# Kernel tuning notes

Hardware: AMD Instinct MI355X
Metric: run time of the kernel (lower is better)

The kernel has to match this reference:

```python
import jax, jax.numpy as jnp
import numpy as np
from jax import lax

SCORE_T = 0.5
NMS_T = 0.7
MAX_DET = 100
B, N = 8, 4096


def _box_cxcywh_to_xyxy(b):
    cx, cy, w, h = jnp.split(b, 4, axis=-1)
    return jnp.concatenate([cx - 0.5 * w, cy - 0.5 * h, cx + 0.5 * w, cy + 0.5 * h], axis=-1)


def _pairwise_iou(b):  # b: [N,4] xyxy -> [N,N]
    area = jnp.clip(b[:, 2] - b[:, 0], 0) * jnp.clip(b[:, 3] - b[:, 1], 0)
    lt = jnp.maximum(b[:, None, :2], b[None, :, :2])
    rb = jnp.minimum(b[:, None, 2:], b[None, :, 2:])
    wh = jnp.clip(rb - lt, 0)
    inter = wh[..., 0] * wh[..., 1]
    union = area[:, None] + area[None, :] - inter
    return inter / jnp.maximum(union, 1e-9)


def _nms_keep(iou, valid):
    # greedy NMS over score-descending order; keep[i]=True means box i survives
    n = valid.shape[0]
    idx = jnp.arange(n)

    def body(i, keep):
        sup = keep[i] & (iou[i] > NMS_T) & (idx > i)
        return keep & ~sup

    return lax.fori_loop(0, n, body, valid)


def _postprocess_image(boxes, scores):
    # boxes: [N,4] cxcywh, scores: [N]
    valid = scores > SCORE_T                       # score filter mask
    order = jnp.argsort(-jnp.where(valid, scores, -jnp.inf))  # score-descending
    bs = boxes[order]
    ss = scores[order]
    vs = valid[order]
    xyxy = _box_cxcywh_to_xyxy(bs)                 # NMS runs on xyxy boxes
    iou = _pairwise_iou(xyxy)
    keep = _nms_keep(lax.stop_gradient(iou), vs)
    kept_scores = jnp.where(keep, ss, -jnp.inf)
    top_s, top_i = lax.top_k(kept_scores, MAX_DET)  # final topk cap
    v = jnp.isfinite(top_s)
    out_boxes = bs[top_i] * v[:, None].astype(bs.dtype)  # original cxcywh boxes, zero-padded
    out_scores = jnp.where(v, top_s, 0.0)
    num = jnp.sum(v.astype(jnp.int32))
    return out_boxes, out_scores, num


def setup_inputs() -> dict:
    key = jax.random.key(0)
    k1, k2 = jax.random.split(key)
    pred_boxes = jax.random.uniform(k1, (B, N, 4), dtype=jnp.float32)
    scores = jax.random.uniform(k2, (B, N), dtype=jnp.float32)
    return {"pred_boxes": pred_boxes, "scores": scores}


def reference(pred_boxes, scores):
    out_boxes, out_scores, num = jax.vmap(_postprocess_image)(pred_boxes, scores)
    # packed [B, MAX_DET, 5]: xyxy-stage-filtered cxcywh boxes + score; num: [B]
    packed = jnp.concatenate([out_boxes, out_scores[..., None]], axis=-1)
    return packed, num
```

## Files before the change

kernel.cpp:

```cpp
#include <hip/hip_runtime.h>

#define NT 1024
#define NW 16
#define NH 4
#define NBOX 4096
#define NPT 4
#define MAXDET 100
#define KSEL 192
#define CAP 512
#define MSMALL 320

typedef unsigned long long u64;
typedef unsigned int u32;
typedef unsigned short u16;

__device__ __forceinline__ float iou_xyxy(float4 a, float4 c) {
  float aa = fmaxf(a.z - a.x, 0.f) * fmaxf(a.w - a.y, 0.f);
  float ca = fmaxf(c.z - c.x, 0.f) * fmaxf(c.w - c.y, 0.f);
  float w = fmaxf(fminf(a.z, c.z) - fmaxf(a.x, c.x), 0.f);
  float h = fmaxf(fminf(a.w, c.w) - fmaxf(a.y, c.y), 0.f);
  float inter = w * h;
  return inter / fmaxf(aa + ca - inter, 1e-9f);
}

__device__ __forceinline__ u64 wave_or64(u64 v) {
#pragma unroll
  for (int d = 1; d < 64; d <<= 1) v |= __shfl_xor(v, d);
  return v;
}

__device__ __forceinline__ u64 serial_greedy(u64 rows_mine, u64 removed) {
  u64 keep = 0ull;
  for (int ii = 0; ii < 64; ++ii) {
    u64 row = __shfl(rows_mine, ii);
    if (!((removed >> ii) & 1ull)) { keep |= 1ull << ii; removed |= row; }
  }
  return keep;
}

template <bool LDSBOX>
__device__ void run_nms128(const u64* keys, int len, const float4* __restrict__ bx,
                           const u16* sortedSlot, const float4* cbst,
                           float4* chbox, float4* chcw, u64* srowLo, u64* srowHi,
                           u64* crossM, u64* keptkey, float4* keptxy, float4* keptcw,
                           int* p_kept, int tid) {
  const int lane = tid & 63;
  for (int base = 0; base < len; base += 128) {
    if (*p_kept >= MAXDET) break;
    const int L = min(128, len - base);
    if (tid < 128) {
      if (tid < 2) crossM[tid] = 0ull;
      float4 bb = make_float4(0.f, 0.f, 0.f, 0.f);
      float4 c = make_float4(0.f, 0.f, 0.f, 0.f);
      if (tid < L) {
        if (LDSBOX) {
          c = cbst[sortedSlot[base + tid]];
        } else {
          u64 k = keys[base + tid];
          int orig = NBOX - 1 - (int)(k & 0xFFFFFFFFull);
          c = bx[orig];
        }
        bb = make_float4(c.x - 0.5f * c.z, c.y - 0.5f * c.w,
                         c.x + 0.5f * c.z, c.y + 0.5f * c.w);
      }
      chbox[tid] = bb;
      chcw[tid] = c;
      srowLo[tid] = 0ull;
      srowHi[tid] = 0ull;
    }
    __syncthreads();
    const int kept0 = *p_kept;
    {
      int i = tid & 127, slice = tid >> 7;
      if (i < L) {
        float4 a = chbox[i];
        bool hit = false;
        for (int k0 = slice; k0 < kept0 && !hit; k0 += 8)
          if (iou_xyxy(a, keptxy[k0]) > 0.7f) hit = true;
        if (hit) atomicOr(&crossM[i >> 6], 1ull << (i & 63));
        u64 blo = 0ull, bhi = 0ull;
        for (int j = i + 1 + slice; j < L; j += 8)
          if (iou_xyxy(a, chbox[j]) > 0.7f) {
            if (j < 64) blo |= 1ull << j; else bhi |= 1ull << (j - 64);
          }
        if (blo) atomicOr(&srowLo[i], blo);
        if (bhi) atomicOr(&srowHi[i], bhi);
      }
    }
    __syncthreads();
    if (tid < 64) {
      u64 remL = crossM[0], remH = crossM[1];
      if (L < 64) remL |= ~((1ull << L) - 1ull);
      if (L <= 64) remH = ~0ull;
      else if (L < 128) remH |= ~((1ull << (L - 64)) - 1ull);
      u64 rAlo = srowLo[lane], rAhi = srowHi[lane];
      u64 rBhi = srowHi[64 + lane];
      u64 K1 = ~remL;
      u64 c1 = wave_or64(((K1 >> lane) & 1ull) ? (rAlo & K1) : 0ull);
      u64 keep1 = (c1 == 0ull) ? K1 : serial_greedy(rAlo, remL);
      u64 remH2 = remH | wave_or64(((keep1 >> lane) & 1ull) ? rAhi : 0ull);
      u64 K2 = ~remH2;
      u64 c2 = wave_or64(((K2 >> lane) & 1ull) ? (rBhi & K2) : 0ull);
      u64 keep2 = (c2 == 0ull) ? K2 : serial_greedy(rBhi, remH2);
      int cnt1 = (int)__popcll(keep1);
      u64 below = (1ull << lane) - 1ull;
      if ((keep1 >> lane) & 1ull) {
        int pos = kept0 + (int)__popcll(keep1 & below);
        if (pos < MAXDET) {
          keptkey[pos] = keys[base + lane];
          keptxy[pos] = chbox[lane];
          keptcw[pos] = chcw[lane];
        }
      }
      if ((keep2 >> lane) & 1ull) {
        int pos = kept0 + cnt1 + (int)__popcll(keep2 & below);
        if (pos < MAXDET) {
          keptkey[pos] = keys[base + 64 + lane];
          keptxy[pos] = chbox[64 + lane];
          keptcw[pos] = chcw[64 + lane];
        }
      }
      if (lane == 0)
        *p_kept = min(MAXDET, kept0 + cnt1 + (int)__popcll(keep2));
    }
    __syncthreads();
  }
}

__global__ __launch_bounds__(NT) void postproc_kernel(
    const float* __restrict__ boxes,
    const float* __restrict__ scores,
    float* __restrict__ out,
    int B) {
  const int b = blockIdx.x;
  const int tid = threadIdx.x, wid = tid >> 6, lane = tid & 63;

  __shared__ u32 hist[NH][256];
  __shared__ u64 cand[CAP];
  __shared__ u64 sortedCand[CAP];
  __shared__ u16 sortedSlot[CAP];
  __shared__ float4 cbst[CAP];
  __shared__ u64 skey[NBOX];
  __shared__ float4 chbox[128];
  __shared__ float4 chcw[128];
  __shared__ u64 srowLo[128], srowHi[128];
  __shared__ u64 crossM[2];
  __shared__ float4 keptxy[MAXDET];
  __shared__ float4 keptcw[MAXDET];
  __shared__ u64 keptkey[MAXDET];
  __shared__ int s_M, s_C, s_kept, s_ovf, s_byte, s_above, s_bcnt;
  __shared__ int s_minP, s_maxP;

  const float* sc = scores + (size_t)b * NBOX;
  const float4* bx = (const float4*)boxes + (size_t)b * NBOX;

  if (tid == 0) {
    s_M = 0; s_C = 0; s_kept = 0; s_ovf = 0;
    s_minP = 0x7FFFFFFF; s_maxP = -1;
  }
  ((u32*)hist)[tid] = 0u;

  u64 key[NPT];
  {
    const int t4 = tid * NPT;
    float4 f0 = *(const float4*)(sc + t4);
    float xs[NPT] = {f0.x, f0.y, f0.z, f0.w};
    int myM = 0, pmin = 0x7FFFFFFF, pmax = -1;
#pragma unroll
    for (int q = 0; q < NPT; ++q) {
      float x = xs[q];
      bool valid = (x > 0.5f);
      u32 bits = __float_as_uint(x);
      key[q] = valid ? (((u64)bits << 32) | (u64)(u32)(NBOX - 1 - (t4 + q))) : 0ull;
      if (valid) {
        int p = (int)(bits >> 23);
        pmin = min(pmin, p); pmax = max(pmax, p); ++myM;
      }
    }
#pragma unroll
    for (int d = 1; d < 64; d <<= 1) {
      myM += __shfl_xor(myM, d);
      pmin = min(pmin, __shfl_xor(pmin, d));
      pmax = max(pmax, __shfl_xor(pmax, d));
    }
    __syncthreads();
    if (lane == 0) {
      atomicAdd(&s_M, myM);
      atomicMin(&s_minP, pmin);
      atomicMax(&s_maxP, pmax);
    }
  }
  __syncthreads();
  const int M = s_M;
  const bool uniformP = (s_minP == s_maxP);
  bool fullpath = false;
  bool usehist = false;
  u32 thr = 0;

  if (M > MSMALL) {
    if (uniformP) {
      usehist = true;
#pragma unroll
      for (int q = 0; q < NPT; ++q)
        if (key[q]) atomicAdd(&hist[wid >> 2][(u32)(key[q] >> 47) & 255u], 1u);
      __syncthreads();
      if (tid < 64) {
        int cc[4];
#pragma unroll
        for (int qq = 0; qq < 4; ++qq) {
          int bin = tid * 4 + qq;
          cc[qq] = (int)(hist[0][bin] + hist[1][bin] + hist[2][bin] + hist[3][bin]);
        }
        int tot = cc[0] + cc[1] + cc[2] + cc[3];
        int suf = tot;
#pragma unroll
        for (int d = 1; d < 64; d <<= 1) {
          int o = __shfl_down(suf, d);
          if (tid + d < 64) suf += o;
        }
        if (suf - tot < KSEL && suf >= KSEL) {
          int cum = suf - tot;
          for (int qq = 3; qq >= 0; --qq) {
            if (cum + cc[qq] >= KSEL) { s_byte = tid * 4 + qq; s_above = cum; s_bcnt = cc[qq]; break; }
            cum += cc[qq];
          }
        }
      }
      __syncthreads();
      thr = (u32)s_byte;
      if (s_above + s_bcnt > CAP) fullpath = true;
    } else {
      fullpath = true;
    }
  }

  if (!fullpath) {
#pragma unroll
    for (int q = 0; q < NPT; ++q) {
      bool take = key[q] && (!usehist || (((u32)(key[q] >> 47) & 255u) >= thr));
      u64 bal = __ballot(take);
      if (bal) {
        int leader = __ffsll((unsigned long long)bal) - 1;
        int basep = 0;
        if (lane == leader) basep = atomicAdd(&s_C, (int)__popcll(bal));
        basep = __shfl(basep, leader);
        if (take) {
          int pos = basep + (int)__popcll(bal & ((1ull << lane) - 1ull));
          if (pos < CAP) cand[pos] = key[q];
          else s_ovf = 1;
        }
      }
    }
  }
  __syncthreads();
  const int C = min(s_C, CAP);
  if (s_ovf) fullpath = true;

  if (!fullpath && C > 0) {
    float4 gbox;
    const bool hasg = (tid < C);
    if (hasg) {
      u64 k = cand[tid];
      int orig = NBOX - 1 - (int)(k & 0xFFFFFFFFull);
      gbox = bx[orig];
    }
    {
      int i = tid >> 2, sl = tid & 3;
      if (i < C) {
        u64 ki = cand[i];
        int cnt = 0;
        for (int j = sl; j < C; j += 4) cnt += (cand[j] > ki) ? 1 : 0;
        cnt += __shfl_xor(cnt, 1);
        cnt += __shfl_xor(cnt, 2);
        if (sl == 0) { sortedCand[cnt] = ki; sortedSlot[cnt] = (u16)i; }
      }
    }
    if (hasg) cbst[tid] = gbox;
    __syncthreads();
    run_nms128<true>(sortedCand, C, bx, sortedSlot, cbst, chbox, chcw,
                     srowLo, srowHi, crossM, keptkey, keptxy, keptcw, &s_kept, tid);
  }

  const int kept1 = s_kept;
  const bool selDropped = usehist && (C < M);
  const bool need_full = fullpath || (kept1 < MAXDET && selDropped);
  __syncthreads();
  if (need_full) {
    if (tid == 0) s_kept = 0;
#pragma unroll
    for (int q = 0; q < NPT; ++q) {
      int n = tid * NPT + q;
      skey[n] = key[q] ? key[q] : (u64)(u32)(NBOX - 1 - n);
    }
    __syncthreads();
    for (int k = 2; k <= NBOX; k <<= 1)
      for (int j = k >> 1; j > 0; j >>= 1) {
#pragma clang loop unroll(disable)
        for (int t = tid; t < NBOX; t += NT) {
          int ixj = t ^ j;
          if (ixj > t) {
            u64 a = skey[t], c2 = skey[ixj];
            bool up = (t & k) != 0;
            if (up ? (a > c2) : (a < c2)) { skey[t] = c2; skey[ixj] = a; }
          }
        }
        __syncthreads();
      }
    run_nms128<false>(skey, s_M, bx, sortedSlot, cbst, chbox, chcw,
                      srowLo, srowHi, crossM, keptkey, keptxy, keptcw, &s_kept, tid);
  }

  const int nk = s_kept;
  if (tid < MAXDET) {
    float v0 = 0.f, v1 = 0.f, v2 = 0.f, v3 = 0.f, v4 = 0.f;
    if (tid < nk) {
      float4 bb = keptcw[tid];
      v0 = bb.x; v1 = bb.y; v2 = bb.z; v3 = bb.w;
      v4 = __uint_as_float((u32)(keptkey[tid] >> 32));
    }
    float* o = out + ((size_t)b * MAXDET + tid) * 5;
    o[0] = v0; o[1] = v1; o[2] = v2; o[3] = v3; o[4] = v4;
  }
  if (tid == 0) out[(size_t)B * MAXDET * 5 + b] = (float)nk;
}

extern "C" void kernel_launch(void* const* d_in, const int* in_sizes, int n_in,
                              void* d_out, int out_size, void* d_ws, size_t ws_size,
                              hipStream_t stream) {
  const float* boxes = (const float*)d_in[0];
  const float* scores = (const float*)d_in[1];
  float* out = (float*)d_out;
  (void)d_ws; (void)ws_size; (void)n_in;
  const int B = out_size / (MAXDET * 5 + 1);
  postproc_kernel<<<B, NT, 0, stream>>>(boxes, scores, out, B);
}
```

Before: 23.85 us.

## Build score histogram in first pass and scatter sorted boxes directly

```diff
diff --git a/kernel.cpp b/kernel.cpp
--- a/kernel.cpp
+++ b/kernel.cpp
@@ -7,12 +7,10 @@
 #define NPT 4
 #define MAXDET 100
 #define KSEL 192
-#define CAP 512
-#define MSMALL 320
+#define CAP 256
 
 typedef unsigned long long u64;
 typedef unsigned int u32;
-typedef unsigned short u16;
 
 __device__ __forceinline__ float iou_xyxy(float4 a, float4 c) {
   float aa = fmaxf(a.z - a.x, 0.f) * fmaxf(a.w - a.y, 0.f);
@@ -40,7 +38,7 @@
 
 template <bool LDSBOX>
 __device__ void run_nms128(const u64* keys, int len, const float4* __restrict__ bx,
-                           const u16* sortedSlot, const float4* cbst,
+                           const float4* cbst,
                            float4* chbox, float4* chcw, u64* srowLo, u64* srowHi,
                            u64* crossM, u64* keptkey, float4* keptxy, float4* keptcw,
                            int* p_kept, int tid) {
@@ -54,7 +52,7 @@
       float4 c = make_float4(0.f, 0.f, 0.f, 0.f);
       if (tid < L) {
         if (LDSBOX) {
-          c = cbst[sortedSlot[base + tid]];
+          c = cbst[base + tid];
         } else {
           u64 k = keys[base + tid];
           int orig = NBOX - 1 - (int)(k & 0xFFFFFFFFull);
@@ -138,7 +136,6 @@
   __shared__ u32 hist[NH][256];
   __shared__ u64 cand[CAP];
   __shared__ u64 sortedCand[CAP];
-  __shared__ u16 sortedSlot[CAP];
   __shared__ float4 cbst[CAP];
   __shared__ u64 skey[NBOX];
   __shared__ float4 chbox[128];
@@ -148,14 +145,15 @@
   __shared__ float4 keptxy[MAXDET];
   __shared__ float4 keptcw[MAXDET];
   __shared__ u64 keptkey[MAXDET];
-  __shared__ int s_M, s_C, s_kept, s_ovf, s_byte, s_above, s_bcnt;
+  __shared__ int s_M, s_C, s_kept, s_byte, s_above, s_bcnt;
   __shared__ int s_minP, s_maxP;
 
   const float* sc = scores + (size_t)b * NBOX;
   const float4* bx = (const float4*)boxes + (size_t)b * NBOX;
 
   if (tid == 0) {
-    s_M = 0; s_C = 0; s_kept = 0; s_ovf = 0;
+    s_C = 0; s_kept = 0;
+    s_byte = 0; s_above = 0; s_bcnt = -1;
     s_minP = 0x7FFFFFFF; s_maxP = -1;
   }
   ((u32*)hist)[tid] = 0u;
@@ -164,8 +162,9 @@
   {
     const int t4 = tid * NPT;
     float4 f0 = *(const float4*)(sc + t4);
+    __syncthreads();
     float xs[NPT] = {f0.x, f0.y, f0.z, f0.w};
-    int myM = 0, pmin = 0x7FFFFFFF, pmax = -1;
+    int pmin = 0x7FFFFFFF, pmax = -1;
 #pragma unroll
     for (int q = 0; q < NPT; ++q) {
       float x = xs[q];
@@ -174,60 +173,53 @@
       key[q] = valid ? (((u64)bits << 32) | (u64)(u32)(NBOX - 1 - (t4 + q))) : 0ull;
       if (valid) {
         int p = (int)(bits >> 23);
-        pmin = min(pmin, p); pmax = max(pmax, p); ++myM;
+        pmin = min(pmin, p); pmax = max(pmax, p);
+        atomicAdd(&hist[wid >> 2][(bits >> 15) & 255u], 1u);
       }
     }
 #pragma unroll
     for (int d = 1; d < 64; d <<= 1) {
-      myM += __shfl_xor(myM, d);
       pmin = min(pmin, __shfl_xor(pmin, d));
       pmax = max(pmax, __shfl_xor(pmax, d));
     }
-    __syncthreads();
     if (lane == 0) {
-      atomicAdd(&s_M, myM);
       atomicMin(&s_minP, pmin);
       atomicMax(&s_maxP, pmax);
+    }
+  }
+  __syncthreads();
+
+  if (tid < 64) {
+    int cc[4];
+#pragma unroll
+    for (int qq = 0; qq < 4; ++qq) {
+      int bin = tid * 4 + qq;
+      cc[qq] = (int)(hist[0][bin] + hist[1][bin] + hist[2][bin] + hist[3][bin]);
+    }
+    int tot = cc[0] + cc[1] + cc[2] + cc[3];
+    int suf = tot;
+#pragma unroll
+    for (int d = 1; d < 64; d <<= 1) {
+      int o = __shfl_down(suf, d);
+      if (tid + d < 64) suf += o;
+    }
+    if (tid == 0) s_M = suf;
+    if (suf - tot < KSEL && suf >= KSEL) {
+      int cum = suf - tot;
+      for (int qq = 3; qq >= 0; --qq) {
+        if (cum + cc[qq] >= KSEL) { s_byte = tid * 4 + qq; s_above = cum; s_bcnt = cc[qq]; break; }
+        cum += cc[qq];
+      }
     }
   }
   __syncthreads();
   const int M = s_M;
   const bool uniformP = (s_minP == s_maxP);
-  bool fullpath = false;
-  bool usehist = false;
-  u32 thr = 0;
-
-  if (M > MSMALL) {
-    if (uniformP) {
+  bool fullpath = false, usehist = false;
+  u32 thr = (u32)s_byte;
+  if (M > CAP) {
+    if (uniformP && s_bcnt >= 0) {
       usehist = true;
-#pragma unroll
-      for (int q = 0; q < NPT; ++q)
-        if (key[q]) atomicAdd(&hist[wid >> 2][(u32)(key[q] >> 47) & 255u], 1u);
-      __syncthreads();
-      if (tid < 64) {
-        int cc[4];
-#pragma unroll
-        for (int qq = 0; qq < 4; ++qq) {
-          int bin = tid * 4 + qq;
-          cc[qq] = (int)(hist[0][bin] + hist[1][bin] + hist[2][bin] + hist[3][bin]);
-        }
-        int tot = cc[0] + cc[1] + cc[2] + cc[3];
-        int suf = tot;
-#pragma unroll
-        for (int d = 1; d < 64; d <<= 1) {
-          int o = __shfl_down(suf, d);
-          if (tid + d < 64) suf += o;
-        }
-        if (suf - tot < KSEL && suf >= KSEL) {
-          int cum = suf - tot;
-          for (int qq = 3; qq >= 0; --qq) {
-            if (cum + cc[qq] >= KSEL) { s_byte = tid * 4 + qq; s_above = cum; s_bcnt = cc[qq]; break; }
-            cum += cc[qq];
-          }
-        }
-      }
-      __syncthreads();
-      thr = (u32)s_byte;
       if (s_above + s_bcnt > CAP) fullpath = true;
     } else {
       fullpath = true;
@@ -246,44 +238,37 @@
         basep = __shfl(basep, leader);
         if (take) {
           int pos = basep + (int)__popcll(bal & ((1ull << lane) - 1ull));
-          if (pos < CAP) cand[pos] = key[q];
-          else s_ovf = 1;
+          cand[pos] = key[q];
         }
       }
     }
   }
   __syncthreads();
-  const int C = min(s_C, CAP);
-  if (s_ovf) fullpath = true;
+  const int C = s_C;
 
   if (!fullpath && C > 0) {
+    const int i = tid >> 2, sl = tid & 3;
+    u64 ki = 0ull;
     float4 gbox;
-    const bool hasg = (tid < C);
-    if (hasg) {
-      u64 k = cand[tid];
-      int orig = NBOX - 1 - (int)(k & 0xFFFFFFFFull);
+    const bool own = (sl == 0) && (i < C);
+    if (i < C) ki = cand[i];
+    if (own) {
+      int orig = NBOX - 1 - (int)(ki & 0xFFFFFFFFull);
       gbox = bx[orig];
     }
-    {
-      int i = tid >> 2, sl = tid & 3;
-      if (i < C) {
-        u64 ki = cand[i];
-        int cnt = 0;
-        for (int j = sl; j < C; j += 4) cnt += (cand[j] > ki) ? 1 : 0;
-        cnt += __shfl_xor(cnt, 1);
-        cnt += __shfl_xor(cnt, 2);
-        if (sl == 0) { sortedCand[cnt] = ki; sortedSlot[cnt] = (u16)i; }
-      }
-    }
-    if (hasg) cbst[tid] = gbox;
-    __syncthreads();
-    run_nms128<true>(sortedCand, C, bx, sortedSlot, cbst, chbox, chcw,
+    int cnt = 0;
+    if (i < C)
+      for (int j = sl; j < C; j += 4) cnt += (cand[j] > ki) ? 1 : 0;
+    cnt += __shfl_xor(cnt, 1);
+    cnt += __shfl_xor(cnt, 2);
+    if (own) { sortedCand[cnt] = ki; cbst[cnt] = gbox; }
+    __syncthreads();
+    run_nms128<true>(sortedCand, C, bx, cbst, chbox, chcw,
                      srowLo, srowHi, crossM, keptkey, keptxy, keptcw, &s_kept, tid);
   }
 
   const int kept1 = s_kept;
-  const bool selDropped = usehist && (C < M);
-  const bool need_full = fullpath || (kept1 < MAXDET && selDropped);
+  const bool need_full = fullpath || (kept1 < MAXDET && usehist && C < M);
   __syncthreads();
   if (need_full) {
     if (tid == 0) s_kept = 0;
@@ -306,7 +291,7 @@
         }
         __syncthreads();
       }
-    run_nms128<false>(skey, s_M, bx, sortedSlot, cbst, chbox, chcw,
+    run_nms128<false>(skey, M, bx, cbst, chbox, chcw,
                       srowLo, srowHi, crossM, keptkey, keptxy, keptcw, &s_kept, tid);
   }
 
```

Result: slower. 25.27 us (+6.0%).
